# Optimization experiments

Measured on AMD Instinct MI355X. Metric: run time of the kernel, lower is better.

## Reference

```python
import jax, jax.numpy as jnp
import numpy as np

B, T, D = 16, 2048, 256

def setup_inputs() -> dict:
    key = jax.random.key(0)
    k1, k2, k3 = jax.random.split(key, 3)
    q = jax.random.normal(k1, (B, T, D), dtype=jnp.float32)
    a = jax.random.normal(k2, (B, T, D), dtype=jnp.float32)
    # original uses 'uniform' init; scale ~ small
    U = jax.random.uniform(k3, (D, D), dtype=jnp.float32, minval=-0.05, maxval=0.05)
    return {"q": q, "a": a, "U": U}

def reference(q, a, U):
    # G[b,i,j] = tanh( (q[b,i,:] @ U) . a[b,j,:] )
    qU = jnp.einsum('btd,de->bte', q, U)                 # [B,Tq,D]
    G = jnp.tanh(jnp.einsum('btd,bsd->bts', qU, a))      # [B,Tq,Ta]
    g_q = jax.nn.softmax(jnp.max(G, axis=-1), axis=1)    # [B,Tq]
    g_a = jax.nn.softmax(jnp.max(G, axis=1), axis=1)     # [B,Ta]
    q_out = jnp.einsum('btd,bt->bd', q, g_q)             # [B,D]
    a_out = jnp.einsum('bsd,bs->bd', a, g_a)             # [B,D]
    return (q_out, a_out)
```

## Files before the change

### kernel.cpp

```cpp
#include <hip/hip_runtime.h>
#include <stdint.h>

typedef __attribute__((ext_vector_type(8))) short s8v;
typedef __attribute__((ext_vector_type(4))) float f4v;

__device__ __forceinline__ unsigned short f2bf(float f) {
  unsigned u = __float_as_uint(f);
  u = u + 0x7FFFu + ((u >> 16) & 1u);
  return (unsigned short)(u >> 16);
}
__device__ __forceinline__ unsigned encf(float f) {
  unsigned i = __float_as_uint(f);
  return (i & 0x80000000u) ? ~i : (i | 0x80000000u);
}
__device__ __forceinline__ float decf(unsigned u) {
  unsigned i = (u & 0x80000000u) ? (u & 0x7FFFFFFFu) : ~u;
  return __uint_as_float(i);
}
__device__ __forceinline__ void gload_lds16(const unsigned short* g, unsigned short* l) {
  __builtin_amdgcn_global_load_lds((const __attribute__((address_space(1))) void*)g,
                                   (__attribute__((address_space(3))) void*)l, 16, 0, 0);
}

__global__ void convert_kernel(const float4* __restrict__ q, const float4* __restrict__ a,
                               const float* __restrict__ U,
                               ushort4* __restrict__ qb, ushort4* __restrict__ ab,
                               unsigned short* __restrict__ Ut,
                               unsigned* __restrict__ rcmax, float* __restrict__ out) {
  const int bx = blockIdx.x;
  if (bx < 8192) {
    const int i = bx * 256 + threadIdx.x;
    float4 v = q[i];
    qb[i] = make_ushort4(f2bf(v.x), f2bf(v.y), f2bf(v.z), f2bf(v.w));
    float4 w = a[i];
    ab[i] = make_ushort4(f2bf(w.x), f2bf(w.y), f2bf(w.z), f2bf(w.w));
  } else if (bx < 8256) {
    const int idx = (bx - 8192) * 256 + threadIdx.x;
    const int n  = idx >> 6;
    const int k4 = (idx & 63) * 4;
    ushort4 o;
    o.x = f2bf(U[(k4 + 0) * 256 + n]);
    o.y = f2bf(U[(k4 + 1) * 256 + n]);
    o.z = f2bf(U[(k4 + 2) * 256 + n]);
    o.w = f2bf(U[(k4 + 3) * 256 + n]);
    *(ushort4*)&Ut[n * 256 + k4] = o;
  } else if (bx < 8320) {
    const int idx = (bx - 8256) * 256 + threadIdx.x;
    *(uint4*)&rcmax[idx * 4] = make_uint4(0u, 0u, 0u, 0u);
  } else {
    out[(bx - 8320) * 256 + threadIdx.x] = 0.f;
  }
}

__global__ __launch_bounds__(512, 2)
void fused_qu_smax(const unsigned short* __restrict__ qb,
                   const unsigned short* __restrict__ Ut,
                   const unsigned short* __restrict__ ab,
                   unsigned* __restrict__ rowmax,
                   unsigned* __restrict__ colmax) {
  extern __shared__ char smem[];
  unsigned short* qUs    = (unsigned short*)smem;
  unsigned short* Bs2    = (unsigned short*)(smem + 65536);
  unsigned*       colLds = (unsigned*)(smem + 131072);
  unsigned*       rowLds = (unsigned*)(smem + 139264);

  const int tid = threadIdx.x;
  const int b = blockIdx.x, tm = blockIdx.y;

  const int lane = tid & 63;
  const int m16  = lane & 15;
  const int quad = lane >> 4;
  const int wave = tid >> 6;
  const int wm   = wave >> 2;
  const int wn   = wave & 3;
  const int srow = tid >> 3;
  const int scol = (((tid & 7) ^ (srow & 7))) * 8;

  #pragma unroll
  for (int i = 0; i < 4; ++i) colLds[i * 512 + tid] = 0u;
  if (tid < 128) rowLds[tid] = 0u;

  const unsigned short* Aq = qb + ((long)b * 2048 + tm * 128) * 256;
  unsigned short* S1 = Bs2;
  unsigned short* S2 = Bs2 + 8192;
  {
    f4v acc[4][4] = {};
    for (int kt = 0; kt < 4; ++kt) {
      const int k0 = kt * 64;
      __syncthreads();
      #pragma unroll
      for (int i = 0; i < 2; ++i)
        gload_lds16(Aq + (long)(i * 64 + srow) * 256 + k0 + scol, &S1[i * 4096 + tid * 8]);
      #pragma unroll
      for (int i = 0; i < 4; ++i)
        gload_lds16(Ut + (long)(i * 64 + srow) * 256 + k0 + scol, &S2[i * 4096 + tid * 8]);
      __syncthreads();
      #pragma unroll
      for (int kk = 0; kk < 2; ++kk) {
        const int cs = ((kk * 4 + quad) ^ (m16 & 7)) * 8;
        s8v af[4], bfv[4];
        #pragma unroll
        for (int i = 0; i < 4; ++i)
          af[i] = *(const s8v*)&S1[(wm * 64 + i * 16 + m16) * 64 + cs];
        #pragma unroll
        for (int j = 0; j < 4; ++j)
          bfv[j] = *(const s8v*)&S2[(wn * 64 + j * 16 + m16) * 64 + cs];
        #pragma unroll
        for (int i = 0; i < 4; ++i)
          #pragma unroll
          for (int j = 0; j < 4; ++j)
            acc[i][j] = __builtin_amdgcn_mfma_f32_16x16x32_bf16(af[i], bfv[j], acc[i][j], 0, 0, 0);
      }
    }
    #pragma unroll
    for (int i = 0; i < 4; ++i)
      #pragma unroll
      for (int r = 0; r < 4; ++r) {
        const int lr = wm * 64 + i * 16 + quad * 4 + r;
        #pragma unroll
        for (int j = 0; j < 4; ++j) {
          const int col = wn * 64 + j * 16 + m16;
          const int ch = (col >> 3) ^ (lr & 7);
          qUs[lr * 256 + ch * 8 + (col & 7)] = f2bf(acc[i][j][r]);
        }
      }
  }
  __syncthreads();

  const unsigned short* Ab_ = ab + (long)b * 2048 * 256;
  float rmx[4][4];
  #pragma unroll
  for (int i = 0; i < 4; ++i)
    #pragma unroll
    for (int r = 0; r < 4; ++r) rmx[i][r] = -3.4e38f;

  #pragma unroll 1
  for (int tb = 0; tb < 16; ++tb) {
    #pragma unroll
    for (int e = 0; e < 8; ++e) {
      const int u = e * 512 + tid;
      const int row = u >> 5;
      const int chs = (u & 31) ^ (row & 7);
      gload_lds16(Ab_ + (long)(tb * 128 + row) * 256 + chs * 8, &Bs2[u * 8]);
    }
    __syncthreads();
    f4v acc[4][2] = {};
    #pragma unroll
    for (int kq = 0; kq < 8; ++kq) {
      const int cs = ((kq * 4 + quad) ^ (m16 & 7)) * 8;
      s8v af[4], bfv[2];
      #pragma unroll
      for (int i = 0; i < 4; ++i)
        af[i] = *(const s8v*)&qUs[(wm * 64 + i * 16 + m16) * 256 + cs];
      #pragma unroll
      for (int j = 0; j < 2; ++j)
        bfv[j] = *(const s8v*)&Bs2[(wn * 32 + j * 16 + m16) * 256 + cs];
      #pragma unroll
      for (int i = 0; i < 4; ++i)
        #pragma unroll
        for (int j = 0; j < 2; ++j)
          acc[i][j] = __builtin_amdgcn_mfma_f32_16x16x32_bf16(af[i], bfv[j], acc[i][j], 0, 0, 0);
    }
    #pragma unroll
    for (int i = 0; i < 4; ++i)
      #pragma unroll
      for (int r = 0; r < 4; ++r)
        rmx[i][r] = fmaxf(rmx[i][r], fmaxf(acc[i][0][r], acc[i][1][r]));
    #pragma unroll
    for (int j = 0; j < 2; ++j) {
      float v = -3.4e38f;
      #pragma unroll
      for (int i = 0; i < 4; ++i)
        #pragma unroll
        for (int r = 0; r < 4; ++r) v = fmaxf(v, acc[i][j][r]);
      v = fmaxf(v, __shfl_xor(v, 16));
      v = fmaxf(v, __shfl_xor(v, 32));
      if (quad == 0) atomicMax(&colLds[tb * 128 + wn * 32 + j * 16 + m16], encf(v));
    }
    __syncthreads();
  }

  #pragma unroll
  for (int i = 0; i < 4; ++i)
    #pragma unroll
    for (int r = 0; r < 4; ++r) {
      float v = rmx[i][r];
      #pragma unroll
      for (int d2 = 1; d2 < 16; d2 <<= 1) v = fmaxf(v, __shfl_xor(v, d2));
      if (m16 == 0) atomicMax(&rowLds[wm * 64 + i * 16 + quad * 4 + r], encf(v));
    }
  __syncthreads();
  if (tid < 128)
    rowmax[(long)b * 2048 + tm * 128 + tid] = rowLds[tid];
  #pragma unroll
  for (int i = 0; i < 4; ++i)
    atomicMax(&colmax[(long)b * 2048 + i * 512 + tid], colLds[i * 512 + tid]);
}

__global__ void wsum_kernel(const uint4* __restrict__ qb, const uint4* __restrict__ ab,
                            const unsigned* __restrict__ rowmax, const unsigned* __restrict__ colmax,
                            float* __restrict__ out) {
  const int tid = threadIdx.x;
  const int chunk = blockIdx.x;
  const int b = blockIdx.y;
  const int z = blockIdx.z;
  const unsigned* e = z ? colmax : rowmax;
  const uint4* src = z ? ab : qb;

  __shared__ float sm[4];
  __shared__ float ss[4];
  __shared__ float wLds[128];
  __shared__ float red[256 * 8];

  float x[8];
  float m = -3.4e38f;
  #pragma unroll
  for (int j = 0; j < 8; ++j) {
    x[j] = tanhf(decf(e[b * 2048 + j * 256 + tid]));
    m = fmaxf(m, x[j]);
  }
  #pragma unroll
  for (int d2 = 1; d2 < 64; d2 <<= 1) m = fmaxf(m, __shfl_xor(m, d2));
  if ((tid & 63) == 0) sm[tid >> 6] = m;
  __syncthreads();
  m = fmaxf(fmaxf(sm[0], sm[1]), fmaxf(sm[2], sm[3]));
  float s = 0.f;
  #pragma unroll
  for (int j = 0; j < 8; ++j) s += expf(x[j] - m);
  #pragma unroll
  for (int d2 = 1; d2 < 64; d2 <<= 1) s += __shfl_xor(s, d2);
  if ((tid & 63) == 0) ss[tid >> 6] = s;
  __syncthreads();
  const float inv = 1.f / (ss[0] + ss[1] + ss[2] + ss[3]);

  if (tid < 128) {
    float xv = tanhf(decf(e[b * 2048 + chunk * 128 + tid]));
    wLds[tid] = expf(xv - m) * inv;
  }
  __syncthreads();

  const int dg = tid & 31;
  const int rg = tid >> 5;
  float acc[8] = {};
  const long rowbase = (long)b * 2048 + chunk * 128;
  for (int t = rg; t < 128; t += 8) {
    const float wgt = wLds[t];
    uint4 v = src[(rowbase + t) * 32 + dg];
    acc[0] += wgt * __uint_as_float(v.x << 16);
    acc[1] += wgt * __uint_as_float(v.x & 0xFFFF0000u);
    acc[2] += wgt * __uint_as_float(v.y << 16);
    acc[3] += wgt * __uint_as_float(v.y & 0xFFFF0000u);
    acc[4] += wgt * __uint_as_float(v.z << 16);
    acc[5] += wgt * __uint_as_float(v.z & 0xFFFF0000u);
    acc[6] += wgt * __uint_as_float(v.w << 16);
    acc[7] += wgt * __uint_as_float(v.w & 0xFFFF0000u);
  }
  #pragma unroll
  for (int k = 0; k < 8; ++k) red[tid * 8 + k] = acc[k];
  __syncthreads();
  if (tid < 32) {
    #pragma unroll
    for (int k = 0; k < 8; ++k) {
      float v = 0.f;
      #pragma unroll
      for (int g = 0; g < 8; ++g) v += red[((g << 5) | tid) * 8 + k];
      atomicAdd(&out[z * 4096 + b * 256 + tid * 8 + k], v);
    }
  }
}

extern "C" void kernel_launch(void* const* d_in, const int* in_sizes, int n_in,
                              void* d_out, int out_size, void* d_ws, size_t ws_size,
                              hipStream_t stream) {
  const float* q = (const float*)d_in[0];
  const float* a = (const float*)d_in[1];
  const float* U = (const float*)d_in[2];
  float* out = (float*)d_out;

  char* w = (char*)d_ws;
  unsigned short* qb = (unsigned short*)w;
  unsigned short* ab = (unsigned short*)(w + (16ull << 20));
  unsigned short* Ut = (unsigned short*)(w + (32ull << 20));
  unsigned* rmax = (unsigned*)(w + (32ull << 20) + (128ull << 10));
  unsigned* cmax = rmax + 32768;

  constexpr int SMEM = 139776;
  hipFuncSetAttribute((const void*)fused_qu_smax,
                      hipFuncAttributeMaxDynamicSharedMemorySize, SMEM);

  convert_kernel<<<8352, 256, 0, stream>>>((const float4*)q, (const float4*)a, U,
                                           (ushort4*)qb, (ushort4*)ab, Ut, rmax, out);

  fused_qu_smax<<<dim3(16, 16), 512, SMEM, stream>>>(qb, Ut, ab, rmax, cmax);

  wsum_kernel<<<dim3(16, 16, 2), 256, 0, stream>>>((const uint4*)qb, (const uint4*)ab,
                                                   rmax, cmax, out);
}
```

Before: 165.7 us.

## Double-buffer A tiles through reused qU LDS and keep qU fragments in registers

Loads the qU A-operand fragments into registers once, then reuses the qU LDS region as a second staging buffer so global-to-LDS loads of the next A tile overlap the MFMA compute on the current one. Manual vmcnt waits and raw barriers replace the full __syncthreads per tile. This removes the exposed global load latency and the repeated LDS reads of qU each tile, at the cost of 32 extra VGPR vectors (higher register pressure, possibly lower occupancy) and fragile waitcnt bookkeeping.

```diff
diff --git a/kernel.cpp b/kernel.cpp
--- a/kernel.cpp
+++ b/kernel.cpp
@@ -128,38 +128,50 @@
   __syncthreads();
 
   const unsigned short* Ab_ = ab + (long)b * 2048 * 256;
-  float rmx[4][4];
-  #pragma unroll
-  for (int i = 0; i < 4; ++i)
-    #pragma unroll
-    for (int r = 0; r < 4; ++r) rmx[i][r] = -3.4e38f;
-
-  #pragma unroll 1
-  for (int tb = 0; tb < 16; ++tb) {
+
+  auto stage = [&](int tb, unsigned short* dst) {
     #pragma unroll
     for (int e = 0; e < 8; ++e) {
       const int u = e * 512 + tid;
       const int row = u >> 5;
       const int chs = (u & 31) ^ (row & 7);
-      gload_lds16(Ab_ + (long)(tb * 128 + row) * 256 + chs * 8, &Bs2[u * 8]);
-    }
-    __syncthreads();
+      gload_lds16(Ab_ + (long)(tb * 128 + row) * 256 + chs * 8, &dst[u * 8]);
+    }
+  };
+
+  stage(0, Bs2);
+
+  s8v aq[4][8];
+  #pragma unroll
+  for (int kq = 0; kq < 8; ++kq) {
+    const int cs = ((kq * 4 + quad) ^ (m16 & 7)) * 8;
+    #pragma unroll
+    for (int i = 0; i < 4; ++i)
+      aq[i][kq] = *(const s8v*)&qUs[(wm * 64 + i * 16 + m16) * 256 + cs];
+  }
+  asm volatile("s_waitcnt lgkmcnt(0)" ::: "memory");
+  __builtin_amdgcn_s_barrier();
+
+  float rmx[4][4];
+  #pragma unroll
+  for (int i = 0; i < 4; ++i)
+    #pragma unroll
+    for (int r = 0; r < 4; ++r) rmx[i][r] = -3.4e38f;
+
+  auto compute = [&](int tb, const unsigned short* buf) {
     f4v acc[4][2] = {};
     #pragma unroll
     for (int kq = 0; kq < 8; ++kq) {
       const int cs = ((kq * 4 + quad) ^ (m16 & 7)) * 8;
-      s8v af[4], bfv[2];
+      s8v bfv[2];
+      #pragma unroll
+      for (int j = 0; j < 2; ++j)
+        bfv[j] = *(const s8v*)&buf[(wn * 32 + j * 16 + m16) * 256 + cs];
       #pragma unroll
       for (int i = 0; i < 4; ++i)
-        af[i] = *(const s8v*)&qUs[(wm * 64 + i * 16 + m16) * 256 + cs];
-      #pragma unroll
-      for (int j = 0; j < 2; ++j)
-        bfv[j] = *(const s8v*)&Bs2[(wn * 32 + j * 16 + m16) * 256 + cs];
-      #pragma unroll
-      for (int i = 0; i < 4; ++i)
         #pragma unroll
         for (int j = 0; j < 2; ++j)
-          acc[i][j] = __builtin_amdgcn_mfma_f32_16x16x32_bf16(af[i], bfv[j], acc[i][j], 0, 0, 0);
+          acc[i][j] = __builtin_amdgcn_mfma_f32_16x16x32_bf16(aq[i][kq], bfv[j], acc[i][j], 0, 0, 0);
     }
     #pragma unroll
     for (int i = 0; i < 4; ++i)
@@ -177,7 +189,25 @@
       v = fmaxf(v, __shfl_xor(v, 32));
       if (quad == 0) atomicMax(&colLds[tb * 128 + wn * 32 + j * 16 + m16], encf(v));
     }
-    __syncthreads();
+  };
+
+  #pragma unroll 1
+  for (int t2 = 0; t2 < 8; ++t2) {
+    const int te = t2 * 2;
+    stage(te + 1, qUs);
+    asm volatile("s_waitcnt vmcnt(8)" ::: "memory");
+    __builtin_amdgcn_s_barrier();
+    compute(te, Bs2);
+    __builtin_amdgcn_s_barrier();
+    if (te + 2 < 16) {
+      stage(te + 2, Bs2);
+      asm volatile("s_waitcnt vmcnt(8)" ::: "memory");
+    } else {
+      asm volatile("s_waitcnt vmcnt(0)" ::: "memory");
+    }
+    __builtin_amdgcn_s_barrier();
+    compute(te + 1, qUs);
+    __builtin_amdgcn_s_barrier();
   }
 
   #pragma unroll
```

Result: slower. 188.2 us (+13.6%).

## Keep qU fragments in registers and read a tiles directly from global memory

Applied to the files above, without the earlier changes.

The second GEMM phase now loads each wave's 32-row slice of qU into registers once, before the loop over a tiles, instead of re-reading it from LDS every tile. The per-tile LDS staging of a through global_load_lds is removed, and each wave reads its B fragments straight from global memory. Per-tile __syncthreads become bare s_barrier calls. The wave tiling changes from 64x32 to 32x64. This cuts LDS traffic and block-wide synchronisation, at the cost of uncoalesced, latency-exposed global loads on the MFMA critical path and higher register pressure.

```diff
diff --git a/kernel.cpp b/kernel.cpp
--- a/kernel.cpp
+++ b/kernel.cpp
@@ -52,7 +52,7 @@
   }
 }
 
-__global__ __launch_bounds__(512, 2)
+__global__ __attribute__((amdgpu_flat_work_group_size(512, 512), amdgpu_waves_per_eu(2, 2)))
 void fused_qu_smax(const unsigned short* __restrict__ qb,
                    const unsigned short* __restrict__ Ut,
                    const unsigned short* __restrict__ ab,
@@ -73,6 +73,8 @@
   const int wave = tid >> 6;
   const int wm   = wave >> 2;
   const int wn   = wave & 3;
+  const int wr32 = (wave >> 1) * 32;
+  const int wc64 = (wave & 1) * 64;
   const int srow = tid >> 3;
   const int scol = (((tid & 7) ^ (srow & 7))) * 8;
 
@@ -128,66 +130,68 @@
   __syncthreads();
 
   const unsigned short* Ab_ = ab + (long)b * 2048 * 256;
-  float rmx[4][4];
-  #pragma unroll
-  for (int i = 0; i < 4; ++i)
+
+  s8v aq[2][8];
+  #pragma unroll
+  for (int kq = 0; kq < 8; ++kq) {
+    const int cs = ((kq * 4 + quad) ^ (m16 & 7)) * 8;
+    aq[0][kq] = *(const s8v*)&qUs[(wr32 + m16) * 256 + cs];
+    aq[1][kq] = *(const s8v*)&qUs[(wr32 + 16 + m16) * 256 + cs];
+  }
+
+  float rmx[2][4];
+  #pragma unroll
+  for (int i = 0; i < 2; ++i)
     #pragma unroll
     for (int r = 0; r < 4; ++r) rmx[i][r] = -3.4e38f;
 
   #pragma unroll 1
   for (int tb = 0; tb < 16; ++tb) {
-    #pragma unroll
-    for (int e = 0; e < 8; ++e) {
-      const int u = e * 512 + tid;
-      const int row = u >> 5;
-      const int chs = (u & 31) ^ (row & 7);
-      gload_lds16(Ab_ + (long)(tb * 128 + row) * 256 + chs * 8, &Bs2[u * 8]);
-    }
-    __syncthreads();
-    f4v acc[4][2] = {};
+    __builtin_amdgcn_s_barrier();
+    f4v acc[2][4] = {};
     #pragma unroll
     for (int kq = 0; kq < 8; ++kq) {
-      const int cs = ((kq * 4 + quad) ^ (m16 & 7)) * 8;
-      s8v af[4], bfv[2];
-      #pragma unroll
-      for (int i = 0; i < 4; ++i)
-        af[i] = *(const s8v*)&qUs[(wm * 64 + i * 16 + m16) * 256 + cs];
-      #pragma unroll
-      for (int j = 0; j < 2; ++j)
-        bfv[j] = *(const s8v*)&Bs2[(wn * 32 + j * 16 + m16) * 256 + cs];
-      #pragma unroll
-      for (int i = 0; i < 4; ++i)
-        #pragma unroll
-        for (int j = 0; j < 2; ++j)
-          acc[i][j] = __builtin_amdgcn_mfma_f32_16x16x32_bf16(af[i], bfv[j], acc[i][j], 0, 0, 0);
-    }
-    #pragma unroll
-    for (int i = 0; i < 4; ++i)
+      const unsigned short* gp = Ab_ + (long)(tb * 128 + wc64 + m16) * 256 + kq * 32 + quad * 8;
+      const s8v b0 = *(const s8v*)&gp[0 * 16 * 256];
+      const s8v b1 = *(const s8v*)&gp[1 * 16 * 256];
+      const s8v b2 = *(const s8v*)&gp[2 * 16 * 256];
+      const s8v b3 = *(const s8v*)&gp[3 * 16 * 256];
+      acc[0][0] = __builtin_amdgcn_mfma_f32_16x16x32_bf16(aq[0][kq], b0, acc[0][0], 0, 0, 0);
+      acc[1][0] = __builtin_amdgcn_mfma_f32_16x16x32_bf16(aq[1][kq], b0, acc[1][0], 0, 0, 0);
+      acc[0][1] = __builtin_amdgcn_mfma_f32_16x16x32_bf16(aq[0][kq], b1, acc[0][1], 0, 0, 0);
+      acc[1][1] = __builtin_amdgcn_mfma_f32_16x16x32_bf16(aq[1][kq], b1, acc[1][1], 0, 0, 0);
+      acc[0][2] = __builtin_amdgcn_mfma_f32_16x16x32_bf16(aq[0][kq], b2, acc[0][2], 0, 0, 0);
+      acc[1][2] = __builtin_amdgcn_mfma_f32_16x16x32_bf16(aq[1][kq], b2, acc[1][2], 0, 0, 0);
+      acc[0][3] = __builtin_amdgcn_mfma_f32_16x16x32_bf16(aq[0][kq], b3, acc[0][3], 0, 0, 0);
+      acc[1][3] = __builtin_amdgcn_mfma_f32_16x16x32_bf16(aq[1][kq], b3, acc[1][3], 0, 0, 0);
+    }
+    #pragma unroll
+    for (int i = 0; i < 2; ++i)
       #pragma unroll
       for (int r = 0; r < 4; ++r)
-        rmx[i][r] = fmaxf(rmx[i][r], fmaxf(acc[i][0][r], acc[i][1][r]));
-    #pragma unroll
-    for (int j = 0; j < 2; ++j) {
-      float v = -3.4e38f;
-      #pragma unroll
-      for (int i = 0; i < 4; ++i)
-        #pragma unroll
-        for (int r = 0; r < 4; ++r) v = fmaxf(v, acc[i][j][r]);
+        rmx[i][r] = fmaxf(rmx[i][r],
+          fmaxf(fmaxf(acc[i][0][r], acc[i][1][r]),
+                fmaxf(acc[i][2][r], acc[i][3][r])));
+    #pragma unroll
+    for (int j = 0; j < 4; ++j) {
+      float v = fmaxf(fmaxf(acc[0][j][0], acc[0][j][1]),
+                      fmaxf(acc[0][j][2], acc[0][j][3]));
+      v = fmaxf(v, fmaxf(fmaxf(acc[1][j][0], acc[1][j][1]),
+                         fmaxf(acc[1][j][2], acc[1][j][3])));
       v = fmaxf(v, __shfl_xor(v, 16));
       v = fmaxf(v, __shfl_xor(v, 32));
-      if (quad == 0) atomicMax(&colLds[tb * 128 + wn * 32 + j * 16 + m16], encf(v));
-    }
-    __syncthreads();
-  }
-
-  #pragma unroll
-  for (int i = 0; i < 4; ++i)
+      if (quad == 0) atomicMax(&colLds[tb * 128 + wc64 + j * 16 + m16], encf(v));
+    }
+  }
+
+  #pragma unroll
+  for (int i = 0; i < 2; ++i)
     #pragma unroll
     for (int r = 0; r < 4; ++r) {
       float v = rmx[i][r];
       #pragma unroll
       for (int d2 = 1; d2 < 16; d2 <<= 1) v = fmaxf(v, __shfl_xor(v, d2));
-      if (m16 == 0) atomicMax(&rowLds[wm * 64 + i * 16 + quad * 4 + r], encf(v));
+      if (m16 == 0) atomicMax(&rowLds[wr32 + i * 16 + quad * 4 + r], encf(v));
     }
   __syncthreads();
   if (tid < 128)
```

After: 249.2 us. +50.4%, slower.
